# Performance work log

Measured on AMD Instinct MI355X. Metric: run time of the kernel, lower is better.

Reference implementation:

```python
import jax, jax.numpy as jnp
import numpy as np

M, N = 2048, 128  # m basis operators, n-dim Hilbert space

def setup_inputs() -> dict:
    key = jax.random.key(0)
    k1, k2, k3, k4 = jax.random.split(key, 4)
    return {
        "basis_re": jax.random.normal(k1, (M, N, N), dtype=jnp.float32),
        "basis_im": jax.random.normal(k2, (M, N, N), dtype=jnp.float32),
        "theta": jax.random.uniform(k3, (4, N), dtype=jnp.float32, minval=-1.0, maxval=1.0),
        "evl": jax.random.uniform(k4, (2,), dtype=jnp.float32, minval=-1.0, maxval=1.0),
    }

def reference(basis_re, basis_im, theta, evl):
    m = basis_re.shape[0]
    # basis_orth_conj: conj of basis, flattened to (m, n*n)
    B = (basis_re - 1j * basis_im).reshape(m, -1)
    # first eigenvector
    c0 = theta[0] + 1j * theta[1]
    evc0 = c0 / jnp.linalg.norm(c0)
    # second eigenvector, Gram-Schmidt against evc0 (vdot conjugates 1st arg)
    c1 = theta[2] + 1j * theta[3]
    c1 = c1 - jnp.vdot(evc0, c1) * evc0
    evc1 = c1 / jnp.linalg.norm(c1)
    # eigenvalues: softplus then L2-normalize
    lam = jax.nn.softplus(evl)
    lam = lam / jnp.linalg.norm(lam)
    # rank-2 Hermitian: lam0 * evc0 evc0^H - lam1 * evc1 evc1^H  (n, n)
    matH = evc0[:, None] * (evc0.conj() * lam[0]) - evc1[:, None] * (evc1.conj() * lam[1])
    # (m, n^2) @ (n^2,) complex matvec, then squared L2 norm
    v = B @ matH.reshape(-1)
    return jnp.sum((v.conj() * v).real)
```

## Files before the change

### kernel.cpp

```cpp
#include <hip/hip_runtime.h>

#define N 128
#define NN 16384
#define M 2048


__device__ __forceinline__ float block_reduce128(float v, float* red, int i) {
    __syncthreads();
    red[i] = v;
    __syncthreads();
    for (int off = 64; off > 0; off >>= 1) {
        if (i < off) red[i] += red[i + off];
        __syncthreads();
    }
    return red[0];
}

__global__ void prep_kernel(const float* __restrict__ theta,
                            const float* __restrict__ evl,
                            float* __restrict__ ws) {
    __shared__ float red[N];
    const int i = threadIdx.x;

    float c0r = theta[i], c0i = theta[N + i];
    float s0 = block_reduce128(c0r * c0r + c0i * c0i, red, i);
    float inv0 = rsqrtf(s0);
    float a0r = c0r * inv0, a0i = c0i * inv0;

    float c1r = theta[2 * N + i], c1i = theta[3 * N + i];
    float dr = block_reduce128(a0r * c1r + a0i * c1i, red, i);
    float di = block_reduce128(a0r * c1i - a0i * c1r, red, i);
    c1r -= dr * a0r - di * a0i;
    c1i -= dr * a0i + di * a0r;

    float s1 = block_reduce128(c1r * c1r + c1i * c1i, red, i);
    float inv1 = rsqrtf(s1);
    float a1r = c1r * inv1, a1i = c1i * inv1;

    float l0 = log1pf(expf(evl[0]));
    float l1 = log1pf(expf(evl[1]));
    float inl = rsqrtf(l0 * l0 + l1 * l1);
    l0 *= inl; l1 *= inl;

    float4* E4 = (float4*)ws;
    E4[i]       = make_float4(a0r, a0i, a1r, a1i);
    E4[128 + i] = make_float4(l0 * a0r, l0 * a0i, l1 * a1r, l1 * a1i);
}

__global__ __launch_bounds__(256, 4) void dot_kernel(
        const float4* __restrict__ br, const float4* __restrict__ bi,
        const float* __restrict__ ws, float2* __restrict__ jout) {
    __shared__ __align__(16) float4 sG[N];
    const int t = threadIdx.x;
    if (t < N) sG[t] = ((const float4*)ws)[N + t];

    const int lane = t & 63;
    const int wave = t >> 6;
    const int job  = blockIdx.x * 4 + wave;
    const int k    = job >> 1;
    const float4* __restrict__ src =
        ((job & 1) ? bi : br) + (size_t)k * (NN / 4);

    const int j4 = lane & 31;
    const float4* E4 = (const float4*)ws;
    float4 E0 = E4[4 * j4 + 0];
    float4 E1 = E4[4 * j4 + 1];
    float4 E2 = E4[4 * j4 + 2];
    float4 E3 = E4[4 * j4 + 3];
    const int h = lane >> 5;
    __syncthreads();

    float4 buf[4];
    #pragma unroll
    for (int p = 0; p < 4; ++p) buf[p] = src[64 * p + lane];

    float P = 0.f, Q = 0.f;

#define BODY(a, c)                                                        \
    {                                                                     \
        float4 g = sG[2 * (c) + h];                                       \
        float d0r = a.x * E0.x + a.y * E1.x + a.z * E2.x + a.w * E3.x;    \
        float d0i = a.x * E0.y + a.y * E1.y + a.z * E2.y + a.w * E3.y;    \
        float d1r = a.x * E0.z + a.y * E1.z + a.z * E2.z + a.w * E3.z;    \
        float d1i = a.x * E0.w + a.y * E1.w + a.z * E2.w + a.w * E3.w;    \
        P += g.x * d0r + g.y * d0i - g.z * d1r - g.w * d1i;               \
        Q += g.y * d0r - g.x * d0i - g.w * d1r + g.z * d1i;               \
    }

    int c = 0;
    #pragma unroll 4
    for (; c < 60; ++c) {
        float4 a = buf[c & 3];
        buf[c & 3] = src[64 * (c + 4) + lane];
        BODY(a, c)
    }
    #pragma unroll
    for (; c < 64; ++c) {
        float4 a = buf[c & 3];
        BODY(a, c)
    }
#undef BODY

    for (int off = 32; off > 0; off >>= 1) {
        P += __shfl_down(P, off);
        Q += __shfl_down(Q, off);
    }
    if (lane == 0) jout[job] = make_float2(P, Q);
}

__global__ __launch_bounds__(256) void reduce_kernel(
        const float4* __restrict__ jout4, float* __restrict__ out) {
    const int k = blockIdx.x * 256 + threadIdx.x;
    float4 f = jout4[k];
    float vr = f.x + f.w;
    float vi = f.y - f.z;
    float s = vr * vr + vi * vi;

    for (int off = 32; off > 0; off >>= 1) s += __shfl_down(s, off);
    __shared__ float sw[4];
    const int wave = threadIdx.x >> 6, lane = threadIdx.x & 63;
    if (lane == 0) sw[wave] = s;
    __syncthreads();
    if (threadIdx.x == 0)
        atomicAdd(out, sw[0] + sw[1] + sw[2] + sw[3]);
}

extern "C" void kernel_launch(void* const* d_in, const int* in_sizes, int n_in,
                              void* d_out, int out_size, void* d_ws, size_t ws_size,
                              hipStream_t stream) {
    const float* basis_re = (const float*)d_in[0];
    const float* basis_im = (const float*)d_in[1];
    const float* theta    = (const float*)d_in[2];
    const float* evl      = (const float*)d_in[3];
    float* out = (float*)d_out;
    float* ws  = (float*)d_ws;

    hipMemsetAsync(d_out, 0, sizeof(float), stream);
    prep_kernel<<<1, 128, 0, stream>>>(theta, evl, ws);
    dot_kernel<<<M / 2, 256, 0, stream>>>((const float4*)basis_re,
                                          (const float4*)basis_im,
                                          ws, (float2*)(ws + 1024));
    reduce_kernel<<<8, 256, 0, stream>>>((const float4*)(ws + 1024), out);
}
```

Measured before the change: 290.7 us.

## Spread matvec chunks across many more waves with atomic per-row accumulation

```diff
diff --git a/kernel.cpp b/kernel.cpp
--- a/kernel.cpp
+++ b/kernel.cpp
@@ -3,6 +3,9 @@
 #define N 128
 #define NN 16384
 #define M 2048
+#define CHUNKS 131072
+#define WAVES 8192
+#define STEPS 32
 
 
 __device__ __forceinline__ float block_reduce128(float v, float* red, int i) {
@@ -47,19 +50,17 @@
     E4[128 + i] = make_float4(l0 * a0r, l0 * a0i, l1 * a1r, l1 * a1i);
 }
 
-__global__ __launch_bounds__(256, 4) void dot_kernel(
+__global__ __launch_bounds__(256, 8) void dot_kernel(
         const float4* __restrict__ br, const float4* __restrict__ bi,
-        const float* __restrict__ ws, float2* __restrict__ jout) {
+        const float* __restrict__ ws, float* __restrict__ accR,
+        float* __restrict__ accI) {
     __shared__ __align__(16) float4 sG[N];
     const int t = threadIdx.x;
     if (t < N) sG[t] = ((const float4*)ws)[N + t];
 
     const int lane = t & 63;
     const int wave = t >> 6;
-    const int job  = blockIdx.x * 4 + wave;
-    const int k    = job >> 1;
-    const float4* __restrict__ src =
-        ((job & 1) ? bi : br) + (size_t)k * (NN / 4);
+    const int wgid = blockIdx.x * 4 + wave;
 
     const int j4 = lane & 31;
     const float4* E4 = (const float4*)ws;
@@ -72,48 +73,51 @@
 
     float4 buf[4];
     #pragma unroll
-    for (int p = 0; p < 4; ++p) buf[p] = src[64 * p + lane];
-
-    float P = 0.f, Q = 0.f;
-
-#define BODY(a, c)                                                        \
-    {                                                                     \
-        float4 g = sG[2 * (c) + h];                                       \
-        float d0r = a.x * E0.x + a.y * E1.x + a.z * E2.x + a.w * E3.x;    \
-        float d0i = a.x * E0.y + a.y * E1.y + a.z * E2.y + a.w * E3.y;    \
-        float d1r = a.x * E0.z + a.y * E1.z + a.z * E2.z + a.w * E3.z;    \
-        float d1i = a.x * E0.w + a.y * E1.w + a.z * E2.w + a.w * E3.w;    \
-        P += g.x * d0r + g.y * d0i - g.z * d1r - g.w * d1i;               \
-        Q += g.y * d0r - g.x * d0i - g.w * d1r + g.z * d1i;               \
+    for (int p = 0; p < 4; ++p) {
+        const int cid = wgid + p * WAVES;
+        buf[p] = br[(size_t)cid * 64 + lane];
     }
 
-    int c = 0;
     #pragma unroll 4
-    for (; c < 60; ++c) {
-        float4 a = buf[c & 3];
-        buf[c & 3] = src[64 * (c + 4) + lane];
-        BODY(a, c)
+    for (int s = 0; s < STEPS; ++s) {
+        float4 a = buf[s & 3];
+        if (s < STEPS - 4) {
+            const int pid = wgid + (s + 4) * WAVES;
+            const int aid = pid & (CHUNKS - 1);
+            const float4* base = (pid < CHUNKS) ? br : bi;
+            buf[s & 3] = base[(size_t)aid * 64 + lane];
+        }
+
+        const int cid  = wgid + s * WAVES;
+        const int isRe = (cid < CHUNKS);
+        const int aid  = cid & (CHUNKS - 1);
+        const int k    = aid >> 6;
+        const int lc   = aid & 63;
+
+        float4 g = sG[2 * lc + h];
+        float d0r = a.x * E0.x + a.y * E1.x + a.z * E2.x + a.w * E3.x;
+        float d0i = a.x * E0.y + a.y * E1.y + a.z * E2.y + a.w * E3.y;
+        float d1r = a.x * E0.z + a.y * E1.z + a.z * E2.z + a.w * E3.z;
+        float d1i = a.x * E0.w + a.y * E1.w + a.z * E2.w + a.w * E3.w;
+        float P = g.x * d0r + g.y * d0i - g.z * d1r - g.w * d1i;
+        float Q = g.y * d0r - g.x * d0i - g.w * d1r + g.z * d1i;
+
+        for (int off = 32; off > 0; off >>= 1) {
+            P += __shfl_down(P, off);
+            Q += __shfl_down(Q, off);
+        }
+        if (lane == 0) {
+            atomicAdd(&accR[k], isRe ? P : Q);
+            atomicAdd(&accI[k], isRe ? Q : -P);
+        }
     }
-    #pragma unroll
-    for (; c < 64; ++c) {
-        float4 a = buf[c & 3];
-        BODY(a, c)
-    }
-#undef BODY
-
-    for (int off = 32; off > 0; off >>= 1) {
-        P += __shfl_down(P, off);
-        Q += __shfl_down(Q, off);
-    }
-    if (lane == 0) jout[job] = make_float2(P, Q);
 }
 
 __global__ __launch_bounds__(256) void reduce_kernel(
-        const float4* __restrict__ jout4, float* __restrict__ out) {
+        const float* __restrict__ accR, const float* __restrict__ accI,
+        float* __restrict__ out) {
     const int k = blockIdx.x * 256 + threadIdx.x;
-    float4 f = jout4[k];
-    float vr = f.x + f.w;
-    float vi = f.y - f.z;
+    float vr = accR[k], vi = accI[k];
     float s = vr * vr + vi * vi;
 
     for (int off = 32; off > 0; off >>= 1) s += __shfl_down(s, off);
@@ -136,9 +140,10 @@
     float* ws  = (float*)d_ws;
 
     hipMemsetAsync(d_out, 0, sizeof(float), stream);
+    hipMemsetAsync(ws + 1024, 0, 2 * M * sizeof(float), stream);
     prep_kernel<<<1, 128, 0, stream>>>(theta, evl, ws);
-    dot_kernel<<<M / 2, 256, 0, stream>>>((const float4*)basis_re,
-                                          (const float4*)basis_im,
-                                          ws, (float2*)(ws + 1024));
-    reduce_kernel<<<8, 256, 0, stream>>>((const float4*)(ws + 1024), out);
+    dot_kernel<<<WAVES / 4, 256, 0, stream>>>((const float4*)basis_re,
+                                              (const float4*)basis_im,
+                                              ws, ws + 1024, ws + 1024 + M);
+    reduce_kernel<<<M / 256, 256, 0, stream>>>(ws + 1024, ws + 1024 + M, out);
 }
```

After: 325.0 us. 1.12x slower.
